# Optimization experiments

Hardware: AMD Instinct MI355X
Metric: run time of the kernel (lower is better)

## Reference

```python
import jax, jax.numpy as jnp
import numpy as np

N = 100000   # nodes
E = 400000   # edges
G = 2000     # graphs in batch
F0 = 84      # num_features_xd
F2 = 840     # num_features_xd * 10


def setup_inputs() -> dict:
    key = jax.random.key(0)
    ks = jax.random.split(key, 8)
    x = jax.random.normal(ks[0], (N, F0), dtype=jnp.float32)
    edge_index = jax.random.randint(ks[1], (2, E), 0, N)
    batch = jnp.sort(jax.random.randint(ks[2], (N,), 0, G))

    def lin(k, fan_in, fan_out):
        bound = 1.0 / np.sqrt(fan_in)
        kw, kb = jax.random.split(k)
        W = jax.random.uniform(kw, (fan_in, fan_out), jnp.float32, -bound, bound)
        b = jax.random.uniform(kb, (fan_out,), jnp.float32, -bound, bound)
        return W, b

    W1, b1 = lin(ks[3], F0, F0)          # GINConv.nn of conv1
    W2, b2 = lin(ks[4], F0, F2)          # GINConv.nn of conv2
    Wf1, bf1 = lin(ks[5], 2 * F2, 1024)  # fc_g[0]
    Wf2, bf2 = lin(ks[6], 1024, 384)     # fc_g[3]
    return dict(x=x, edge_index=edge_index, batch=batch,
                W1=W1, b1=b1, W2=W2, b2=b2,
                Wf1=Wf1, bf1=bf1, Wf2=Wf2, bf2=bf2)


def _gin_conv(h, src, dst, W, b):
    # GINConv with default eps=0: nn((1+eps)*h + sum_{j in N(i)} h_j)
    agg = jax.ops.segment_sum(h[src], dst, num_segments=N)  # scatter-add over edges
    return (h + agg) @ W + b


def reference(x, edge_index, batch, W1, b1, W2, b2, Wf1, bf1, Wf2, bf2):
    src, dst = edge_index[0], edge_index[1]
    h1 = jax.nn.relu(_gin_conv(x, src, dst, W1, b1))    # [N, 84]
    h2 = jax.nn.relu(_gin_conv(h1, src, dst, W2, b2))   # [N, 840]
    # global_max_pool / global_add_pool over graphs
    pool_max = jax.ops.segment_max(h2, batch, num_segments=G)  # [G, 840]
    pool_sum = jax.ops.segment_sum(h2, batch, num_segments=G)  # [G, 840]
    xg = jnp.concatenate([pool_max, pool_sum], axis=1)          # [G, 1680]
    # fc_g: Linear->ReLU->(Dropout=id in eval)->Linear
    xg = jax.nn.relu(xg @ Wf1 + bf1) @ Wf2 + bf2                # [G, 384]
    return (xg, h2)
```

## Files before the change

kernel.cpp:

```cpp
#include <hip/hip_runtime.h>
#include <math.h>

#define NN 100000
#define NE 400000
#define NG 2000
#define F0 84
#define F2 840
#define FH 1024
#define FO 384

typedef __attribute__((ext_vector_type(8))) short bf16x8;
typedef __attribute__((ext_vector_type(4))) float f32x4;

__device__ inline short f2bf(float f) {
    union { float f; unsigned u; } v; v.f = f;
    unsigned r = (v.u + 0x7FFFu + ((v.u >> 16) & 1u)) >> 16;
    return (short)r;
}
__device__ inline float b2f(short s) {
    union { unsigned u; float f; } v;
    v.u = ((unsigned)(unsigned short)s) << 16;
    return v.f;
}

__global__ void edge_deg(const int* __restrict__ dst, int* __restrict__ deg) {
    int e = blockIdx.x * blockDim.x + threadIdx.x;
    if (e < NE) atomicAdd(&deg[dst[e]], 1);
}

__global__ void scan_ph1(const int* __restrict__ deg, int* __restrict__ rowptr,
                         int* __restrict__ bsum) {
    __shared__ int s[1024];
    int t = threadIdx.x;
    int i = blockIdx.x * 1024 + t;
    int v = (i < NN) ? deg[i] : 0;
    s[t] = v;
    __syncthreads();
    for (int d = 1; d < 1024; d <<= 1) {
        int u = (t >= d) ? s[t - d] : 0;
        __syncthreads();
        s[t] += u;
        __syncthreads();
    }
    if (i < NN) rowptr[i] = s[t] - v;
    if (t == 1023) bsum[blockIdx.x] = s[t];
}

__global__ void scan_ph2(int* __restrict__ bsum, int nb) {
    __shared__ int s[128];
    int t = threadIdx.x;
    int v = (t < nb) ? bsum[t] : 0;
    s[t] = v;
    __syncthreads();
    for (int d = 1; d < 128; d <<= 1) {
        int u = (t >= d) ? s[t - d] : 0;
        __syncthreads();
        s[t] += u;
        __syncthreads();
    }
    if (t < nb) bsum[t] = s[t] - v;
}

__global__ void scan_ph3(int* __restrict__ rowptr, const int* __restrict__ bsum) {
    int t = threadIdx.x;
    int i = blockIdx.x * 1024 + t;
    if (i < NN) rowptr[i] += bsum[blockIdx.x];
    if (i == 0) rowptr[NN] = NE;
}

__global__ void edge_fill(const int* __restrict__ src, const int* __restrict__ dst,
                          const int* __restrict__ rowptr, int* __restrict__ cnt,
                          int* __restrict__ eid) {
    int e = blockIdx.x * blockDim.x + threadIdx.x;
    if (e >= NE) return;
    int d = dst[e];
    int p = rowptr[d] + atomicAdd(&cnt[d], 1);
    eid[p] = src[e];
}

__global__ void cast_x(const float* __restrict__ x, short* __restrict__ Xb) {
    int idx = blockIdx.x * blockDim.x + threadIdx.x;
    if (idx >= NN * 12) return;
    int n = idx / 12;
    int c = idx - n * 12;
    int k0 = c * 8;
    bf16x8 v;
#pragma unroll
    for (int j = 0; j < 8; ++j) {
        int k = k0 + j;
        v[j] = (k < F0) ? f2bf(x[(size_t)n * F0 + k]) : (short)0;
    }
    *reinterpret_cast<bf16x8*>(Xb + (size_t)n * 96 + k0) = v;
}

__device__ inline void pack_one(const float* __restrict__ W, short* __restrict__ P,
                                int K, int N, int KB, int CT, int idx) {
    int lane = idx & 63;
    int t    = idx >> 6;
    int kb   = t % KB;
    int ct   = t / KB;
    int col  = ct * 16 + (lane & 15);
    int k0   = kb * 32 + ((lane >> 4) << 3);
    bf16x8 v;
#pragma unroll
    for (int j = 0; j < 8; ++j) {
        int k = k0 + j;
        float f = (k < K && col < N) ? W[(size_t)k * N + col] : 0.f;
        v[j] = f2bf(f);
    }
    *reinterpret_cast<bf16x8*>(P + (size_t)idx * 8) = v;
}

#define S1 (6*3*64)
#define S2 (56*3*64)
#define S3 (64*53*64)
#define S4 (24*32*64)
__global__ void pack_all(const float* __restrict__ W1, short* __restrict__ P1,
                         const float* __restrict__ W2, short* __restrict__ P2,
                         const float* __restrict__ Wf1, short* __restrict__ P3,
                         const float* __restrict__ Wf2, short* __restrict__ P4) {
    int idx = blockIdx.x * blockDim.x + threadIdx.x;
    if (idx < S1) { pack_one(W1, P1, F0, F0, 3, 6, idx); return; }
    idx -= S1;
    if (idx < S2) { pack_one(W2, P2, F0, F2, 3, 56, idx); return; }
    idx -= S2;
    if (idx < S3) { pack_one(Wf1, P3, 1680, FH, 53, 64, idx); return; }
    idx -= S3;
    if (idx < S4) { pack_one(Wf2, P4, FH, FO, 32, 24, idx); return; }
}

template <int CTW, int NWAVES, bool OUTBF16>
__global__ void conv_fused(const short* __restrict__ H,
                           const int* __restrict__ rowptr,
                           const int* __restrict__ eid,
                           const short* __restrict__ Bp,
                           const float* __restrict__ bias,
                           void* __restrict__ Cout,
                           int Nbias, int ldc, int ncols) {
    __shared__ short Alds[3 * 512];
    int rt = blockIdx.x;
    int t  = threadIdx.x;

    for (int item = t; item < 192; item += NWAVES * 64) {
        int r = item / 12;
        int c = item - r * 12;
        int n = rt * 16 + r;
        int off = c * 8;
        bf16x8 sv = *reinterpret_cast<const bf16x8*>(H + (size_t)n * 96 + off);
        float acc[8];
#pragma unroll
        for (int j = 0; j < 8; ++j) acc[j] = b2f(sv[j]);
        int e0 = rowptr[n], e1 = rowptr[n + 1];
        for (int e = e0; e < e1; ++e) {
            int s = eid[e];
            bf16x8 v = *reinterpret_cast<const bf16x8*>(H + (size_t)s * 96 + off);
#pragma unroll
            for (int j = 0; j < 8; ++j) acc[j] += b2f(v[j]);
        }
        bf16x8 o;
#pragma unroll
        for (int j = 0; j < 8; ++j) o[j] = f2bf(acc[j]);
        int kb = c >> 2, q = c & 3;
        *reinterpret_cast<bf16x8*>(&Alds[(kb * 512) + (q * 16 + r) * 8]) = o;
    }
    __syncthreads();

    int wave = t >> 6;
    int lane = t & 63;
    f32x4 acc[CTW];
#pragma unroll
    for (int u = 0; u < CTW; ++u) acc[u] = (f32x4){0.f, 0.f, 0.f, 0.f};
    const short* Bbase = Bp + (size_t)(wave * CTW) * 3 * 512 + lane * 8;
#pragma unroll
    for (int kb = 0; kb < 3; ++kb) {
        bf16x8 a = *reinterpret_cast<const bf16x8*>(&Alds[kb * 512 + lane * 8]);
#pragma unroll
        for (int u = 0; u < CTW; ++u) {
            bf16x8 b = *reinterpret_cast<const bf16x8*>(Bbase + ((size_t)u * 3 + kb) * 512);
            acc[u] = __builtin_amdgcn_mfma_f32_16x16x32_bf16(a, b, acc[u], 0, 0, 0);
        }
    }
    int row0 = rt * 16 + ((lane >> 4) << 2);
#pragma unroll
    for (int u = 0; u < CTW; ++u) {
        int col = (wave * CTW + u) * 16 + (lane & 15);
        float bi = (col < Nbias) ? bias[col] : 0.f;
        if (col < ncols) {
#pragma unroll
            for (int r = 0; r < 4; ++r) {
                float v = fmaxf(acc[u][r] + bi, 0.f);
                if (OUTBF16) ((short*)Cout)[(size_t)(row0 + r) * ldc + col] = f2bf(v);
                else         ((float*)Cout)[(size_t)(row0 + r) * ldc + col] = v;
            }
        }
    }
}

template <int CTW, bool RELU, bool OUTBF16>
__global__ void gemmN(const short* __restrict__ A, const short* __restrict__ Bp,
                      const float* __restrict__ bias, void* __restrict__ Cout,
                      int Kp, int Nbias, int ldc, int ncols,
                      int rowTiles, int ctGroups) {
    int gid = blockIdx.x * blockDim.x + threadIdx.x;
    int w   = gid >> 6;
    if (w >= rowTiles * ctGroups) return;
    int lane = gid & 63;
    int rt = w / ctGroups;
    int cg = w - rt * ctGroups;
    int KB = Kp >> 5;
    const short* Ap = A + (size_t)(rt * 16 + (lane & 15)) * Kp + ((lane >> 4) << 3);
    const short* Bbase = Bp + (size_t)(cg * CTW) * KB * 512 + lane * 8;
    f32x4 acc[CTW];
#pragma unroll
    for (int u = 0; u < CTW; ++u) acc[u] = (f32x4){0.f, 0.f, 0.f, 0.f};
    for (int kb = 0; kb < KB; ++kb) {
        bf16x8 a = *reinterpret_cast<const bf16x8*>(Ap + kb * 32);
#pragma unroll
        for (int u = 0; u < CTW; ++u) {
            bf16x8 b = *reinterpret_cast<const bf16x8*>(Bbase + ((size_t)u * KB + kb) * 512);
            acc[u] = __builtin_amdgcn_mfma_f32_16x16x32_bf16(a, b, acc[u], 0, 0, 0);
        }
    }
    int row0 = rt * 16 + ((lane >> 4) << 2);
#pragma unroll
    for (int u = 0; u < CTW; ++u) {
        int col = (cg * CTW + u) * 16 + (lane & 15);
        float bi = (col < Nbias) ? bias[col] : 0.f;
        if (col < ncols) {
#pragma unroll
            for (int r = 0; r < 4; ++r) {
                int row = row0 + r;
                float v = acc[u][r] + bi;
                if (RELU) v = fmaxf(v, 0.f);
                if (OUTBF16) ((short*)Cout)[(size_t)row * ldc + col] = f2bf(v);
                else         ((float*)Cout)[(size_t)row * ldc + col] = v;
            }
        }
    }
}

__global__ void pool_kernel(const float* __restrict__ h2,
                            const int* __restrict__ batch,
                            short* __restrict__ A3) {
    int g = blockIdx.x;
    int t = threadIdx.x;
    __shared__ int se[2];
    if (t < 2) {
        int target = g + t;
        int lo = 0, hi = NN;
        while (lo < hi) {
            int mid = (lo + hi) >> 1;
            if (batch[mid] < target) lo = mid + 1; else hi = mid;
        }
        se[t] = lo;
    }
    __syncthreads();
    int s = se[0], e = se[1];
    if (t < 210) {
        int c4 = t * 4;
        float sm0 = 0.f, sm1 = 0.f, sm2 = 0.f, sm3 = 0.f;
        float mx0 = -INFINITY, mx1 = -INFINITY, mx2 = -INFINITY, mx3 = -INFINITY;
        for (int n = s; n < e; ++n) {
            float4 v = *reinterpret_cast<const float4*>(h2 + (size_t)n * F2 + c4);
            sm0 += v.x; sm1 += v.y; sm2 += v.z; sm3 += v.w;
            mx0 = fmaxf(mx0, v.x); mx1 = fmaxf(mx1, v.y);
            mx2 = fmaxf(mx2, v.z); mx3 = fmaxf(mx3, v.w);
        }
        short* xr = A3 + (size_t)g * 1696;
        short4 mo, so;
        mo.x = f2bf(mx0); mo.y = f2bf(mx1); mo.z = f2bf(mx2); mo.w = f2bf(mx3);
        so.x = f2bf(sm0); so.y = f2bf(sm1); so.z = f2bf(sm2); so.w = f2bf(sm3);
        *reinterpret_cast<short4*>(xr + c4)      = mo;
        *reinterpret_cast<short4*>(xr + F2 + c4) = so;
    }
    if (t >= 210 && t < 214) {
        short4 z = {0, 0, 0, 0};
        *reinterpret_cast<short4*>(A3 + (size_t)g * 1696 + 1680 + (t - 210) * 4) = z;
    }
}

extern "C" void kernel_launch(void* const* d_in, const int* in_sizes, int n_in,
                              void* d_out, int out_size, void* d_ws, size_t ws_size,
                              hipStream_t stream) {
    const float* x    = (const float*)d_in[0];
    const int*   ei   = (const int*)d_in[1];
    const int*   batch= (const int*)d_in[2];
    const float* W1   = (const float*)d_in[3];
    const float* b1   = (const float*)d_in[4];
    const float* W2   = (const float*)d_in[5];
    const float* b2   = (const float*)d_in[6];
    const float* Wf1  = (const float*)d_in[7];
    const float* bf1  = (const float*)d_in[8];
    const float* Wf2  = (const float*)d_in[9];
    const float* bf2  = (const float*)d_in[10];

    const int* src = ei;
    const int* dst = ei + NE;

    float* xg_out = (float*)d_out;
    float* h2     = (float*)d_out + (size_t)NG * FO;

    short* Xb   = (short*)d_ws;
    short* h1   = Xb + (size_t)NN * 96;
    short* A3   = h1 + (size_t)NN * 96;
    short* fc1o = A3 + (size_t)NG * 1696;
    short* W1p  = fc1o + (size_t)NG * FH;
    short* W2p  = W1p + (size_t)S1 * 8;
    short* Wf1p = W2p + (size_t)S2 * 8;
    short* Wf2p = Wf1p + (size_t)S3 * 8;
    int*   deg  = (int*)(Wf2p + (size_t)S4 * 8);
    int*   cnt  = deg + NN;
    int*   rowptr = cnt + NN;
    int*   bsum = rowptr + NN + 1;
    int*   eid  = bsum + 128;

    const int blk = 256;
    auto cdiv = [](long long a, long long b) { return (int)((a + b - 1) / b); };
    const int nb1024 = cdiv(NN, 1024);

    hipMemsetAsync(deg, 0, 2 * (size_t)NN * sizeof(int), stream);
    edge_deg<<<cdiv(NE, blk), blk, 0, stream>>>(dst, deg);
    scan_ph1<<<nb1024, 1024, 0, stream>>>(deg, rowptr, bsum);
    scan_ph2<<<1, 128, 0, stream>>>(bsum, nb1024);
    scan_ph3<<<nb1024, 1024, 0, stream>>>(rowptr, bsum);
    edge_fill<<<cdiv(NE, blk), blk, 0, stream>>>(src, dst, rowptr, cnt, eid);

    pack_all<<<cdiv(S1 + S2 + S3 + S4, blk), blk, 0, stream>>>(
        W1, W1p, W2, W2p, Wf1, Wf1p, Wf2, Wf2p);
    cast_x<<<cdiv((long long)NN * 12, blk), blk, 0, stream>>>(x, Xb);

    conv_fused<6, 1, true><<<6250, 64, 0, stream>>>(
        Xb, rowptr, eid, W1p, b1, h1, F0, 96, 96);

    conv_fused<14, 4, false><<<6250, 256, 0, stream>>>(
        h1, rowptr, eid, W2p, b2, h2, F2, F2, F2);

    pool_kernel<<<NG, blk, 0, stream>>>(h2, batch, A3);

    gemmN<2, true, true><<<cdiv(125LL * 32 * 64, blk), blk, 0, stream>>>(
        A3, Wf1p, bf1, fc1o, 1696, FH, FH, FH, 125, 32);
    gemmN<2, false, false><<<cdiv(125LL * 12 * 64, blk), blk, 0, stream>>>(
        fc1o, Wf2p, bf2, xg_out, 1024, FO, FO, FO, 125, 12);
}
```

Before: 408.6 us.

## Merge preprocessing launches, retile conv kernels and stage FC GEMM inputs in LDS

Merges degree counting, input cast and weight packing into one front kernel, and folds scan phases 2 and 3 into one kernel that reduces the block sums itself. conv1 now handles four row tiles per 256-thread block, and conv2 handles two row tiles per block so each weight load feeds two MFMAs. The FC layers become per-row-tile blocks that stage A in shared memory and give each wave a wide column group. The aim is fewer launches and less redundant weight traffic, at the cost of more registers in conv2 and far fewer blocks in the FC GEMMs.

```diff
diff --git a/kernel.cpp b/kernel.cpp
--- a/kernel.cpp
+++ b/kernel.cpp
@@ -23,75 +23,14 @@
     return v.f;
 }
 
-__global__ void edge_deg(const int* __restrict__ dst, int* __restrict__ deg) {
-    int e = blockIdx.x * blockDim.x + threadIdx.x;
-    if (e < NE) atomicAdd(&deg[dst[e]], 1);
-}
-
-__global__ void scan_ph1(const int* __restrict__ deg, int* __restrict__ rowptr,
-                         int* __restrict__ bsum) {
-    __shared__ int s[1024];
-    int t = threadIdx.x;
-    int i = blockIdx.x * 1024 + t;
-    int v = (i < NN) ? deg[i] : 0;
-    s[t] = v;
-    __syncthreads();
-    for (int d = 1; d < 1024; d <<= 1) {
-        int u = (t >= d) ? s[t - d] : 0;
-        __syncthreads();
-        s[t] += u;
-        __syncthreads();
-    }
-    if (i < NN) rowptr[i] = s[t] - v;
-    if (t == 1023) bsum[blockIdx.x] = s[t];
-}
-
-__global__ void scan_ph2(int* __restrict__ bsum, int nb) {
-    __shared__ int s[128];
-    int t = threadIdx.x;
-    int v = (t < nb) ? bsum[t] : 0;
-    s[t] = v;
-    __syncthreads();
-    for (int d = 1; d < 128; d <<= 1) {
-        int u = (t >= d) ? s[t - d] : 0;
-        __syncthreads();
-        s[t] += u;
-        __syncthreads();
-    }
-    if (t < nb) bsum[t] = s[t] - v;
-}
-
-__global__ void scan_ph3(int* __restrict__ rowptr, const int* __restrict__ bsum) {
-    int t = threadIdx.x;
-    int i = blockIdx.x * 1024 + t;
-    if (i < NN) rowptr[i] += bsum[blockIdx.x];
-    if (i == 0) rowptr[NN] = NE;
-}
-
-__global__ void edge_fill(const int* __restrict__ src, const int* __restrict__ dst,
-                          const int* __restrict__ rowptr, int* __restrict__ cnt,
-                          int* __restrict__ eid) {
-    int e = blockIdx.x * blockDim.x + threadIdx.x;
-    if (e >= NE) return;
-    int d = dst[e];
-    int p = rowptr[d] + atomicAdd(&cnt[d], 1);
-    eid[p] = src[e];
-}
-
-__global__ void cast_x(const float* __restrict__ x, short* __restrict__ Xb) {
-    int idx = blockIdx.x * blockDim.x + threadIdx.x;
-    if (idx >= NN * 12) return;
-    int n = idx / 12;
-    int c = idx - n * 12;
-    int k0 = c * 8;
-    bf16x8 v;
-#pragma unroll
-    for (int j = 0; j < 8; ++j) {
-        int k = k0 + j;
-        v[j] = (k < F0) ? f2bf(x[(size_t)n * F0 + k]) : (short)0;
-    }
-    *reinterpret_cast<bf16x8*>(Xb + (size_t)n * 96 + k0) = v;
-}
+#define S1 (6*3*64)
+#define S2 (56*3*64)
+#define S3 (64*53*64)
+#define S4 (24*32*64)
+#define PACK_TOT (S1 + S2 + S3 + S4)
+#define NB_DEG  1563
+#define NB_CAST 4688
+#define NB_PACK 1087
 
 __device__ inline void pack_one(const float* __restrict__ W, short* __restrict__ P,
                                 int K, int N, int KB, int CT, int idx) {
@@ -111,15 +50,37 @@
     *reinterpret_cast<bf16x8*>(P + (size_t)idx * 8) = v;
 }
 
-#define S1 (6*3*64)
-#define S2 (56*3*64)
-#define S3 (64*53*64)
-#define S4 (24*32*64)
-__global__ void pack_all(const float* __restrict__ W1, short* __restrict__ P1,
-                         const float* __restrict__ W2, short* __restrict__ P2,
-                         const float* __restrict__ Wf1, short* __restrict__ P3,
-                         const float* __restrict__ Wf2, short* __restrict__ P4) {
-    int idx = blockIdx.x * blockDim.x + threadIdx.x;
+__global__ void front_kernel(const int* __restrict__ dst, int* __restrict__ deg,
+                             const float* __restrict__ x, short* __restrict__ Xb,
+                             const float* __restrict__ W1, short* __restrict__ P1,
+                             const float* __restrict__ W2, short* __restrict__ P2,
+                             const float* __restrict__ Wf1, short* __restrict__ P3,
+                             const float* __restrict__ Wf2, short* __restrict__ P4) {
+    int bid = blockIdx.x;
+    if (bid < NB_DEG) {
+        int e = bid * 256 + threadIdx.x;
+        if (e < NE) atomicAdd(&deg[dst[e]], 1);
+        return;
+    }
+    bid -= NB_DEG;
+    if (bid < NB_CAST) {
+        int idx = bid * 256 + threadIdx.x;
+        if (idx < NN * 12) {
+            int n = idx / 12;
+            int c = idx - n * 12;
+            int k0 = c * 8;
+            bf16x8 v;
+#pragma unroll
+            for (int j = 0; j < 8; ++j) {
+                int k = k0 + j;
+                v[j] = (k < F0) ? f2bf(x[(size_t)n * F0 + k]) : (short)0;
+            }
+            *reinterpret_cast<bf16x8*>(Xb + (size_t)n * 96 + k0) = v;
+        }
+        return;
+    }
+    bid -= NB_CAST;
+    int idx = bid * 256 + threadIdx.x;
     if (idx < S1) { pack_one(W1, P1, F0, F0, 3, 6, idx); return; }
     idx -= S1;
     if (idx < S2) { pack_one(W2, P2, F0, F2, 3, 56, idx); return; }
@@ -129,111 +90,164 @@
     if (idx < S4) { pack_one(Wf2, P4, FH, FO, 32, 24, idx); return; }
 }
 
-template <int CTW, int NWAVES, bool OUTBF16>
-__global__ void conv_fused(const short* __restrict__ H,
-                           const int* __restrict__ rowptr,
-                           const int* __restrict__ eid,
-                           const short* __restrict__ Bp,
-                           const float* __restrict__ bias,
-                           void* __restrict__ Cout,
-                           int Nbias, int ldc, int ncols) {
-    __shared__ short Alds[3 * 512];
-    int rt = blockIdx.x;
-    int t  = threadIdx.x;
-
-    for (int item = t; item < 192; item += NWAVES * 64) {
+__global__ void scan_ph1(const int* __restrict__ deg, int* __restrict__ rowptr,
+                         int* __restrict__ bsum) {
+    __shared__ int s[1024];
+    int t = threadIdx.x;
+    int i = blockIdx.x * 1024 + t;
+    int v = (i < NN) ? deg[i] : 0;
+    s[t] = v;
+    __syncthreads();
+    for (int d = 1; d < 1024; d <<= 1) {
+        int u = (t >= d) ? s[t - d] : 0;
+        __syncthreads();
+        s[t] += u;
+        __syncthreads();
+    }
+    if (i < NN) rowptr[i] = s[t] - v;
+    if (t == 1023) bsum[blockIdx.x] = s[t];
+}
+
+__global__ void scan_ph23(int* __restrict__ rowptr, const int* __restrict__ bsum,
+                          int nb) {
+    __shared__ int s[128];
+    int t = threadIdx.x;
+    int b = blockIdx.x;
+    if (t < 128) s[t] = (t < b && t < nb) ? bsum[t] : 0;
+    __syncthreads();
+    for (int d = 64; d >= 1; d >>= 1) {
+        if (t < d) s[t] += s[t + d];
+        __syncthreads();
+    }
+    int off = s[0];
+    int i = b * 1024 + t;
+    if (i < NN) rowptr[i] += off;
+    if (i == 0) rowptr[NN] = NE;
+}
+
+__global__ void edge_fill(const int* __restrict__ src, const int* __restrict__ dst,
+                          const int* __restrict__ rowptr, int* __restrict__ cnt,
+                          int* __restrict__ eid) {
+    int e = blockIdx.x * blockDim.x + threadIdx.x;
+    if (e >= NE) return;
+    int d = dst[e];
+    int p = rowptr[d] + atomicAdd(&cnt[d], 1);
+    eid[p] = src[e];
+}
+
+__device__ inline void gather_item(const short* __restrict__ H,
+                                   const int* __restrict__ rowptr,
+                                   const int* __restrict__ eid,
+                                   int n, int c, short* __restrict__ ldsTile) {
+    int off = c * 8;
+    bf16x8 sv = *reinterpret_cast<const bf16x8*>(H + (size_t)n * 96 + off);
+    float acc[8];
+#pragma unroll
+    for (int j = 0; j < 8; ++j) acc[j] = b2f(sv[j]);
+    int e0 = rowptr[n], e1 = rowptr[n + 1];
+    for (int e = e0; e < e1; ++e) {
+        int s = eid[e];
+        bf16x8 v = *reinterpret_cast<const bf16x8*>(H + (size_t)s * 96 + off);
+#pragma unroll
+        for (int j = 0; j < 8; ++j) acc[j] += b2f(v[j]);
+    }
+    bf16x8 o;
+#pragma unroll
+    for (int j = 0; j < 8; ++j) o[j] = f2bf(acc[j]);
+    int kb = c >> 2, q = c & 3;
+    *reinterpret_cast<bf16x8*>(&ldsTile[kb * 512 + (q * 16 + (n & 15)) * 8]) = o;
+}
+
+__global__ __launch_bounds__(256) void conv1_fused(
+        const short* __restrict__ H, const int* __restrict__ rowptr,
+        const int* __restrict__ eid, const short* __restrict__ Bp,
+        const float* __restrict__ bias, short* __restrict__ Cout) {
+    __shared__ short Alds[4][3 * 512];
+    int t = threadIdx.x;
+    int base = blockIdx.x * 64;
+    for (int item = t; item < 768; item += 256) {
         int r = item / 12;
         int c = item - r * 12;
-        int n = rt * 16 + r;
-        int off = c * 8;
-        bf16x8 sv = *reinterpret_cast<const bf16x8*>(H + (size_t)n * 96 + off);
-        float acc[8];
-#pragma unroll
-        for (int j = 0; j < 8; ++j) acc[j] = b2f(sv[j]);
-        int e0 = rowptr[n], e1 = rowptr[n + 1];
-        for (int e = e0; e < e1; ++e) {
-            int s = eid[e];
-            bf16x8 v = *reinterpret_cast<const bf16x8*>(H + (size_t)s * 96 + off);
-#pragma unroll
-            for (int j = 0; j < 8; ++j) acc[j] += b2f(v[j]);
-        }
-        bf16x8 o;
-#pragma unroll
-        for (int j = 0; j < 8; ++j) o[j] = f2bf(acc[j]);
-        int kb = c >> 2, q = c & 3;
-        *reinterpret_cast<bf16x8*>(&Alds[(kb * 512) + (q * 16 + r) * 8]) = o;
-    }
-    __syncthreads();
-
-    int wave = t >> 6;
-    int lane = t & 63;
-    f32x4 acc[CTW];
-#pragma unroll
-    for (int u = 0; u < CTW; ++u) acc[u] = (f32x4){0.f, 0.f, 0.f, 0.f};
-    const short* Bbase = Bp + (size_t)(wave * CTW) * 3 * 512 + lane * 8;
+        int n = base + r;
+        if (n < NN) gather_item(H, rowptr, eid, n, c, Alds[r >> 4]);
+    }
+    __syncthreads();
+    int wave = t >> 6, lane = t & 63;
+    int rt = blockIdx.x * 4 + wave;
+    if (rt >= NN / 16) return;
+    f32x4 acc[6];
+#pragma unroll
+    for (int u = 0; u < 6; ++u) acc[u] = (f32x4){0.f, 0.f, 0.f, 0.f};
+    const short* Bbase = Bp + lane * 8;
 #pragma unroll
     for (int kb = 0; kb < 3; ++kb) {
-        bf16x8 a = *reinterpret_cast<const bf16x8*>(&Alds[kb * 512 + lane * 8]);
-#pragma unroll
-        for (int u = 0; u < CTW; ++u) {
-            bf16x8 b = *reinterpret_cast<const bf16x8*>(Bbase + ((size_t)u * 3 + kb) * 512);
+        bf16x8 a = *reinterpret_cast<const bf16x8*>(&Alds[wave][kb * 512 + lane * 8]);
+#pragma unroll
+        for (int u = 0; u < 6; ++u) {
+            bf16x8 b = *reinterpret_cast<const bf16x8*>(Bbase + ((size_t)(u * 3 + kb)) * 512);
             acc[u] = __builtin_amdgcn_mfma_f32_16x16x32_bf16(a, b, acc[u], 0, 0, 0);
         }
     }
     int row0 = rt * 16 + ((lane >> 4) << 2);
 #pragma unroll
-    for (int u = 0; u < CTW; ++u) {
-        int col = (wave * CTW + u) * 16 + (lane & 15);
-        float bi = (col < Nbias) ? bias[col] : 0.f;
-        if (col < ncols) {
+    for (int u = 0; u < 6; ++u) {
+        int col = u * 16 + (lane & 15);
+        float bi = (col < F0) ? bias[col] : 0.f;
+#pragma unroll
+        for (int r = 0; r < 4; ++r) {
+            float v = fmaxf(acc[u][r] + bi, 0.f);
+            Cout[(size_t)(row0 + r) * 96 + col] = f2bf(v);
+        }
+    }
+}
+
+__global__ __launch_bounds__(256) void conv2_fused(
+        const short* __restrict__ H, const int* __restrict__ rowptr,
+        const int* __restrict__ eid, const short* __restrict__ Bp,
+        const float* __restrict__ bias, float* __restrict__ Cout) {
+    __shared__ short Alds[2][3 * 512];
+    int t = threadIdx.x;
+    int base = blockIdx.x * 32;
+    for (int item = t; item < 384; item += 256) {
+        int r = item / 12;
+        int c = item - r * 12;
+        gather_item(H, rowptr, eid, base + r, c, Alds[r >> 4]);
+    }
+    __syncthreads();
+    int wave = t >> 6, lane = t & 63;
+    f32x4 acc0[14], acc1[14];
+#pragma unroll
+    for (int u = 0; u < 14; ++u) {
+        acc0[u] = (f32x4){0.f, 0.f, 0.f, 0.f};
+        acc1[u] = (f32x4){0.f, 0.f, 0.f, 0.f};
+    }
+    const short* Bbase = Bp + (size_t)(wave * 14) * 3 * 512 + lane * 8;
+#pragma unroll
+    for (int kb = 0; kb < 3; ++kb) {
+        bf16x8 a0 = *reinterpret_cast<const bf16x8*>(&Alds[0][kb * 512 + lane * 8]);
+        bf16x8 a1 = *reinterpret_cast<const bf16x8*>(&Alds[1][kb * 512 + lane * 8]);
+#pragma unroll
+        for (int u = 0; u < 14; ++u) {
+            bf16x8 b = *reinterpret_cast<const bf16x8*>(Bbase + ((size_t)(u * 3 + kb)) * 512);
+            acc0[u] = __builtin_amdgcn_mfma_f32_16x16x32_bf16(a0, b, acc0[u], 0, 0, 0);
+            acc1[u] = __builtin_amdgcn_mfma_f32_16x16x32_bf16(a1, b, acc1[u], 0, 0, 0);
+        }
+    }
+    int rb0 = base + ((lane >> 4) << 2);
+#pragma unroll
+    for (int u = 0; u < 14; ++u) {
+        int col = (wave * 14 + u) * 16 + (lane & 15);
+        if (col < F2) {
+            float bi = bias[col];
 #pragma unroll
             for (int r = 0; r < 4; ++r) {
-                float v = fmaxf(acc[u][r] + bi, 0.f);
-                if (OUTBF16) ((short*)Cout)[(size_t)(row0 + r) * ldc + col] = f2bf(v);
-                else         ((float*)Cout)[(size_t)(row0 + r) * ldc + col] = v;
+                float v = fmaxf(acc0[u][r] + bi, 0.f);
+                Cout[(size_t)(rb0 + r) * F2 + col] = v;
             }
-        }
-    }
-}
-
-template <int CTW, bool RELU, bool OUTBF16>
-__global__ void gemmN(const short* __restrict__ A, const short* __restrict__ Bp,
-                      const float* __restrict__ bias, void* __restrict__ Cout,
-                      int Kp, int Nbias, int ldc, int ncols,
-                      int rowTiles, int ctGroups) {
-    int gid = blockIdx.x * blockDim.x + threadIdx.x;
-    int w   = gid >> 6;
-    if (w >= rowTiles * ctGroups) return;
-    int lane = gid & 63;
-    int rt = w / ctGroups;
-    int cg = w - rt * ctGroups;
-    int KB = Kp >> 5;
-    const short* Ap = A + (size_t)(rt * 16 + (lane & 15)) * Kp + ((lane >> 4) << 3);
-    const short* Bbase = Bp + (size_t)(cg * CTW) * KB * 512 + lane * 8;
-    f32x4 acc[CTW];
-#pragma unroll
-    for (int u = 0; u < CTW; ++u) acc[u] = (f32x4){0.f, 0.f, 0.f, 0.f};
-    for (int kb = 0; kb < KB; ++kb) {
-        bf16x8 a = *reinterpret_cast<const bf16x8*>(Ap + kb * 32);
-#pragma unroll
-        for (int u = 0; u < CTW; ++u) {
-            bf16x8 b = *reinterpret_cast<const bf16x8*>(Bbase + ((size_t)u * KB + kb) * 512);
-            acc[u] = __builtin_amdgcn_mfma_f32_16x16x32_bf16(a, b, acc[u], 0, 0, 0);
-        }
-    }
-    int row0 = rt * 16 + ((lane >> 4) << 2);
-#pragma unroll
-    for (int u = 0; u < CTW; ++u) {
-        int col = (cg * CTW + u) * 16 + (lane & 15);
-        float bi = (col < Nbias) ? bias[col] : 0.f;
-        if (col < ncols) {
 #pragma unroll
             for (int r = 0; r < 4; ++r) {
-                int row = row0 + r;
-                float v = acc[u][r] + bi;
-                if (RELU) v = fmaxf(v, 0.f);
-                if (OUTBF16) ((short*)Cout)[(size_t)row * ldc + col] = f2bf(v);
-                else         ((float*)Cout)[(size_t)row * ldc + col] = v;
+                float v = fmaxf(acc1[u][r] + bi, 0.f);
+                Cout[(size_t)(rb0 + 16 + r) * F2 + col] = v;
             }
         }
     }
@@ -276,6 +290,85 @@
     if (t >= 210 && t < 214) {
         short4 z = {0, 0, 0, 0};
         *reinterpret_cast<short4*>(A3 + (size_t)g * 1696 + 1680 + (t - 210) * 4) = z;
+    }
+}
+
+__global__ __launch_bounds__(256) void fc1_lds(const short* __restrict__ A3,
+                                               const short* __restrict__ Bp,
+                                               const float* __restrict__ bias,
+                                               short* __restrict__ out) {
+    __shared__ short Al[53 * 64 * 8];
+    int t = threadIdx.x;
+    int rt = blockIdx.x;
+    for (int i = t; i < 53 * 64; i += 256) {
+        int lane = i & 63, kb = i >> 6;
+        int row = lane & 15, k0 = kb * 32 + ((lane >> 4) << 3);
+        *reinterpret_cast<bf16x8*>(&Al[i * 8]) =
+            *reinterpret_cast<const bf16x8*>(A3 + (size_t)(rt * 16 + row) * 1696 + k0);
+    }
+    __syncthreads();
+    int wave = t >> 6, lane = t & 63;
+    f32x4 acc[16];
+#pragma unroll
+    for (int u = 0; u < 16; ++u) acc[u] = (f32x4){0.f, 0.f, 0.f, 0.f};
+    const short* Bbase = Bp + (size_t)(wave * 16) * 53 * 512 + lane * 8;
+    for (int kb = 0; kb < 53; ++kb) {
+        bf16x8 a = *reinterpret_cast<const bf16x8*>(&Al[(kb * 64 + lane) * 8]);
+#pragma unroll
+        for (int u = 0; u < 16; ++u) {
+            bf16x8 b = *reinterpret_cast<const bf16x8*>(Bbase + ((size_t)(u * 53 + kb)) * 512);
+            acc[u] = __builtin_amdgcn_mfma_f32_16x16x32_bf16(a, b, acc[u], 0, 0, 0);
+        }
+    }
+    int row0 = rt * 16 + ((lane >> 4) << 2);
+#pragma unroll
+    for (int u = 0; u < 16; ++u) {
+        int col = (wave * 16 + u) * 16 + (lane & 15);
+        float bi = bias[col];
+#pragma unroll
+        for (int r = 0; r < 4; ++r) {
+            float v = fmaxf(acc[u][r] + bi, 0.f);
+            out[(size_t)(row0 + r) * FH + col] = f2bf(v);
+        }
+    }
+}
+
+__global__ __launch_bounds__(256) void fc2_lds(const short* __restrict__ A,
+                                               const short* __restrict__ Bp,
+                                               const float* __restrict__ bias,
+                                               float* __restrict__ out) {
+    __shared__ short Al[32 * 64 * 8];
+    int t = threadIdx.x;
+    int rt = blockIdx.x;
+    for (int i = t; i < 32 * 64; i += 256) {
+        int lane = i & 63, kb = i >> 6;
+        int row = lane & 15, k0 = kb * 32 + ((lane >> 4) << 3);
+        *reinterpret_cast<bf16x8*>(&Al[i * 8]) =
+            *reinterpret_cast<const bf16x8*>(A + (size_t)(rt * 16 + row) * FH + k0);
+    }
+    __syncthreads();
+    int wave = t >> 6, lane = t & 63;
+    f32x4 acc[6];
+#pragma unroll
+    for (int u = 0; u < 6; ++u) acc[u] = (f32x4){0.f, 0.f, 0.f, 0.f};
+    const short* Bbase = Bp + (size_t)(wave * 6) * 32 * 512 + lane * 8;
+    for (int kb = 0; kb < 32; ++kb) {
+        bf16x8 a = *reinterpret_cast<const bf16x8*>(&Al[(kb * 64 + lane) * 8]);
+#pragma unroll
+        for (int u = 0; u < 6; ++u) {
+            bf16x8 b = *reinterpret_cast<const bf16x8*>(Bbase + ((size_t)(u * 32 + kb)) * 512);
+            acc[u] = __builtin_amdgcn_mfma_f32_16x16x32_bf16(a, b, acc[u], 0, 0, 0);
+        }
+    }
+    int row0 = rt * 16 + ((lane >> 4) << 2);
+#pragma unroll
+    for (int u = 0; u < 6; ++u) {
+        int col = (wave * 6 + u) * 16 + (lane & 15);
+        float bi = bias[col];
+#pragma unroll
+        for (int r = 0; r < 4; ++r) {
+            out[(size_t)(row0 + r) * FO + col] = acc[u][r] + bi;
+        }
     }
 }
 
@@ -319,26 +412,19 @@
     const int nb1024 = cdiv(NN, 1024);
 
     hipMemsetAsync(deg, 0, 2 * (size_t)NN * sizeof(int), stream);
-    edge_deg<<<cdiv(NE, blk), blk, 0, stream>>>(dst, deg);
+    front_kernel<<<NB_DEG + NB_CAST + NB_PACK, blk, 0, stream>>>(
+        dst, deg, x, Xb, W1, W1p, W2, W2p, Wf1, Wf1p, Wf2, Wf2p);
+
     scan_ph1<<<nb1024, 1024, 0, stream>>>(deg, rowptr, bsum);
-    scan_ph2<<<1, 128, 0, stream>>>(bsum, nb1024);
-    scan_ph3<<<nb1024, 1024, 0, stream>>>(rowptr, bsum);
+    scan_ph23<<<nb1024, 1024, 0, stream>>>(rowptr, bsum, nb1024);
     edge_fill<<<cdiv(NE, blk), blk, 0, stream>>>(src, dst, rowptr, cnt, eid);
 
-    pack_all<<<cdiv(S1 + S2 + S3 + S4, blk), blk, 0, stream>>>(
-        W1, W1p, W2, W2p, Wf1, Wf1p, Wf2, Wf2p);
-    cast_x<<<cdiv((long long)NN * 12, blk), blk, 0, stream>>>(x, Xb);
-
-    conv_fused<6, 1, true><<<6250, 64, 0, stream>>>(
-        Xb, rowptr, eid, W1p, b1, h1, F0, 96, 96);
-
-    conv_fused<14, 4, false><<<6250, 256, 0, stream>>>(
-        h1, rowptr, eid, W2p, b2, h2, F2, F2, F2);
+    conv1_fused<<<cdiv(NN, 64), blk, 0, stream>>>(Xb, rowptr, eid, W1p, b1, h1);
+
+    conv2_fused<<<NN / 32, blk, 0, stream>>>(h1, rowptr, eid, W2p, b2, h2);
 
     pool_kernel<<<NG, blk, 0, stream>>>(h2, batch, A3);
 
-    gemmN<2, true, true><<<cdiv(125LL * 32 * 64, blk), blk, 0, stream>>>(
-        A3, Wf1p, bf1, fc1o, 1696, FH, FH, FH, 125, 32);
-    gemmN<2, false, false><<<cdiv(125LL * 12 * 64, blk), blk, 0, stream>>>(
-        fc1o, Wf2p, bf2, xg_out, 1024, FO, FO, FO, 125, 12);
-}
+    fc1_lds<<<NG / 16, blk, 0, stream>>>(A3, Wf1p, bf1, fc1o);
+    fc2_lds<<<NG / 16, blk, 0, stream>>>(fc1o, Wf2p, bf2, xg_out);
+}
```

New measurement: 476.7 us. +16.7%, slower.
